# Kernel tuning notes

Measured on AMD Instinct MI355X. Metric: run time of the kernel, lower is better.

The kernel has to match this reference:

```python
import jax, jax.numpy as jnp
import numpy as np

K = 100
TEMPERATURE = 1.0


def setup_inputs() -> dict:
    key = jax.random.key(0)
    k1, k2, k3 = jax.random.split(key, 3)
    student_emb = jax.random.normal(k1, (8, 512, 1500), dtype=jnp.float32)
    teacher_codes = jax.random.randint(k2, (8, 1500), 0, 4096, dtype=jnp.int64)
    codebook = jax.random.normal(k3, (4096, 512), dtype=jnp.float32)
    return {"student_emb": student_emb, "teacher_codes": teacher_codes, "codebook": codebook}


def reference(student_emb, teacher_codes, codebook):
    B, C, T = student_emb.shape
    # flatten tokens: (N, C) with N = B*T
    emb = jnp.transpose(student_emb, (0, 2, 1)).reshape(-1, C)
    codes = teacher_codes.reshape(-1).astype(jnp.int32)

    # Euclidean cdist via the ||a||^2 + ||b||^2 - 2ab expansion (same math as torch.cdist)
    emb_sq = jnp.sum(emb * emb, axis=1, keepdims=True)            # (N,1)
    cb_sq = jnp.sum(codebook * codebook, axis=1)[None, :]         # (1,V)
    d2 = emb_sq + cb_sq - 2.0 * jnp.matmul(emb, codebook.T)       # (N,V)
    distances = jnp.sqrt(jnp.maximum(d2, 0.0))

    # top-k smallest distances
    _, top_k_indices = jax.lax.top_k(-distances, K)               # (N,K)

    # include_correct: replace last candidate with the true code if absent
    correct_in_topk = jnp.any(top_k_indices == codes[:, None], axis=1)
    top_k_indices = top_k_indices.at[:, -1].set(
        jnp.where(correct_in_topk, top_k_indices[:, -1], codes))

    candidate_distances = jnp.take_along_axis(distances, top_k_indices, axis=1)
    logits = -candidate_distances / TEMPERATURE                   # (N,K)

    match = top_k_indices == codes[:, None]
    local_labels = jnp.argmax(match.astype(jnp.int32), axis=1)    # (N,)

    logp = jax.nn.log_softmax(logits, axis=1)
    loss = -jnp.mean(jnp.take_along_axis(logp, local_labels[:, None], axis=1))

    local_predictions = jnp.argmax(logits, axis=-1)
    local_accuracy = jnp.mean((local_predictions == local_labels).astype(jnp.float32))
    global_predictions = jnp.argmin(distances, axis=-1)
    global_accuracy = jnp.mean((global_predictions == codes).astype(jnp.float32))
    correct_in_candidates = jnp.mean(jnp.any(top_k_indices == codes[:, None], axis=1).astype(jnp.float32))

    return loss, local_accuracy, global_accuracy, correct_in_candidates
```

## Files before the change

### kernel.cpp

```cpp
#include <hip/hip_runtime.h>
#include <hip/hip_bf16.h>
#include <cstdint>

#define B_ 8
#define C_ 512
#define T_ 1500
#define N_ (B_*T_)
#define NPAD_ 12032
#define V_ 4096
#define K_ 100
#define BKg 64

typedef unsigned long long u64;
typedef __attribute__((ext_vector_type(8))) short short8;
typedef __attribute__((ext_vector_type(4))) float f32x4;

__device__ __forceinline__ unsigned short f2bf(float x){
    __hip_bfloat16 h = __float2bfloat16(x);
    return __builtin_bit_cast(unsigned short, h);
}
__device__ __forceinline__ unsigned short f2h(float x){
    return __builtin_bit_cast(unsigned short, (_Float16)x);
}
__device__ __forceinline__ float h2fu(unsigned v){
    return (float)__builtin_bit_cast(_Float16, (unsigned short)v);
}

__device__ __forceinline__ void gll16(const unsigned short* g, unsigned short* l){
    __builtin_amdgcn_global_load_lds(
        (const __attribute__((address_space(1))) void*)g,
        (__attribute__((address_space(3))) void*)l, 16, 0, 0);
}

__global__ __launch_bounds__(256) void cbconv_kernel(const float* __restrict__ CB,
                                                     unsigned short* __restrict__ CBh,
                                                     float* __restrict__ csq){
    int wv = threadIdx.x >> 6, lane = threadIdx.x & 63;
    int r = blockIdx.x * 4 + wv;
    const float4* p4 = (const float4*)(CB + (size_t)r * C_);
    ushort4* o4 = (ushort4*)(CBh + (size_t)r * C_);
    float s = 0.f;
    #pragma unroll
    for (int j = 0; j < 2; ++j){
        float4 v = p4[lane + j*64];
        s += v.x*v.x + v.y*v.y + v.z*v.z + v.w*v.w;
        ushort4 h; h.x = f2bf(v.x); h.y = f2bf(v.y); h.z = f2bf(v.z); h.w = f2bf(v.w);
        o4[lane + j*64] = h;
    }
    #pragma unroll
    for (int o = 32; o; o >>= 1) s += __shfl_down(s, o, 64);
    if (lane == 0) csq[r] = s;
}

__global__ __launch_bounds__(256) void transpose_conv_kernel(const float* __restrict__ S,
                                                             unsigned short* __restrict__ embT,
                                                             float* __restrict__ esq){
    __shared__ float tile[32][33];
    __shared__ float psum[8][33];
    int b  = blockIdx.z;
    int c0 = blockIdx.y * 32;
    int t0 = blockIdx.x * 32;
    int tx = threadIdx.x, ty = threadIdx.y;
    #pragma unroll
    for (int r = 0; r < 4; ++r){
        int c = c0 + ty + r*8;
        int t = t0 + tx;
        tile[ty + r*8][tx] = (t < T_) ? S[((size_t)b*C_ + c)*T_ + t] : 0.f;
    }
    __syncthreads();
    float ps = 0.f;
    #pragma unroll
    for (int r = 0; r < 4; ++r){ float v = tile[ty + r*8][tx]; ps += v * v; }
    psum[ty][tx] = ps;
    #pragma unroll
    for (int r = 0; r < 4; ++r){
        int t = t0 + ty + r*8;
        int c = c0 + tx;
        if (t < T_) embT[((size_t)b*T_ + t)*C_ + c] = f2bf(tile[tx][ty + r*8]);
    }
    __syncthreads();
    if (ty == 0){
        int t = t0 + tx;
        if (t < T_){
            float s2 = 0.f;
            #pragma unroll
            for (int w = 0; w < 8; ++w) s2 += psum[w][tx];
            atomicAdd(&esq[b*T_ + t], s2);
        }
    }
}

__global__ __launch_bounds__(256) void gemm_d2h_kernel(
    const unsigned short* __restrict__ A, const unsigned short* __restrict__ Bm,
    const float* __restrict__ esq, const float* __restrict__ csq,
    unsigned short* __restrict__ d2h, int row_lo, int row_hi)
{
    __shared__ unsigned short As[128*BKg];
    __shared__ unsigned short Bs[128*BKg];
    int tid = threadIdx.x, lane = tid & 63, wv = tid >> 6;
    int row0 = row_lo + blockIdx.x * 128;
    int col0 = blockIdx.y * 128;

    int sr = lane >> 3;
    int sk = (lane & 7) * 8;
    int skx = sk ^ (sr * 8);
    const unsigned short* Apg[4]; const unsigned short* Bpg[4];
    unsigned short* Adg[4]; unsigned short* Bdg[4];
    #pragma unroll
    for (int g = 0; g < 4; ++g){
        int r = wv*32 + g*8 + sr;
        int ar = row0 + r; ar = (ar < N_) ? ar : N_-1;
        Apg[g] = A  + (size_t)ar * C_ + skx;
        Bpg[g] = Bm + (size_t)(col0 + r) * C_ + skx;
        Adg[g] = &As[(wv*32 + g*8) * BKg];
        Bdg[g] = &Bs[(wv*32 + g*8) * BKg];
    }

    int wm = (wv >> 1) * 64, wn = (wv & 1) * 64;
    int fr = lane & 15;
    int fk = (lane >> 4) * 8;
    int xo = (fr & 7) * 8;

    f32x4 acc[4][4];
    #pragma unroll
    for (int i = 0; i < 4; ++i)
        #pragma unroll
        for (int j = 0; j < 4; ++j) acc[i][j] = (f32x4){0.f, 0.f, 0.f, 0.f};

    for (int kt = 0; kt < C_/BKg; ++kt){
        int k0 = kt * BKg;
        #pragma unroll
        for (int g = 0; g < 4; ++g) gll16(Apg[g] + k0, Adg[g]);
        #pragma unroll
        for (int g = 0; g < 4; ++g) gll16(Bpg[g] + k0, Bdg[g]);
        __syncthreads();
        #pragma unroll
        for (int kk = 0; kk < 2; ++kk){
            int fo = (fk + kk*32) ^ xo;
            short8 af[4], bf[4];
            #pragma unroll
            for (int i = 0; i < 4; ++i) af[i] = *(const short8*)&As[(wm + i*16 + fr)*BKg + fo];
            #pragma unroll
            for (int j = 0; j < 4; ++j) bf[j] = *(const short8*)&Bs[(wn + j*16 + fr)*BKg + fo];
            #pragma unroll
            for (int i = 0; i < 4; ++i)
                #pragma unroll
                for (int j = 0; j < 4; ++j)
                    acc[i][j] = __builtin_amdgcn_mfma_f32_16x16x32_bf16(af[i], bf[j], acc[i][j], 0, 0, 0);
        }
        __syncthreads();
    }

    int er = (lane >> 4) * 4;
    int ec = lane & 15;
    #pragma unroll
    for (int i = 0; i < 4; ++i){
        #pragma unroll
        for (int r = 0; r < 4; ++r){
            int n = row0 + wm + i*16 + er + r;
            if (n >= row_hi) continue;
            float en = esq[n];
            size_t base = (size_t)(n - row_lo) * V_;
            #pragma unroll
            for (int j = 0; j < 4; ++j){
                int v = col0 + wn + j*16 + ec;
                float d2 = fmaxf(en + csq[v] - 2.f * acc[i][j][r], 0.f);
                d2h[base + v] = f2h(d2);
            }
        }
    }
}

__global__ __launch_bounds__(256, 2) void select_kernel(const unsigned short* __restrict__ d2h,
                                                        const int* __restrict__ codes,
                                                        float2* __restrict__ pairbuf,
                                                        int row_lo, int nrows){
    int tid = threadIdx.x, lane = tid & 63, wv = tid >> 6;
    int lrow = blockIdx.x * 4 + wv;
    if (lrow >= nrows) return;
    int n = row_lo + lrow;
    const uint4* r4 = (const uint4*)(d2h + (size_t)lrow * V_);

    __shared__ unsigned hist[4][256] __attribute__((aligned(16)));
    __shared__ unsigned coll[4][64];
    __shared__ unsigned collcnt[4];

    unsigned p[32];
    #pragma unroll
    for (int j = 0; j < 8; ++j){
        uint4 q = r4[lane + j*64];
        p[4*j] = q.x; p[4*j+1] = q.y; p[4*j+2] = q.z; p[4*j+3] = q.w;
    }
    int code = codes[n];
    unsigned ucode = (unsigned)d2h[(size_t)lrow * V_ + code];

    unsigned cmin = 0xFFFFFFFFu, kmax = 0u;
    #pragma unroll
    for (int m = 0; m < 32; ++m){
        unsigned idx = 8u*(unsigned)lane + 512u*(unsigned)(m>>2) + 2u*(unsigned)(m&3);
        unsigned cl_ = (p[m] << 16) | idx;
        unsigned ch_ = (p[m] & 0xFFFF0000u) | (idx + 1u);
        unsigned cc = (cl_ < ch_) ? cl_ : ch_;
        if (cc < cmin) cmin = cc;
        unsigned lo = p[m] & 0xFFFFu, hi = p[m] >> 16;
        unsigned mm = (lo > hi) ? lo : hi;
        if (mm > kmax) kmax = mm;
    }
    #pragma unroll
    for (int o = 32; o; o >>= 1){
        unsigned a = (unsigned)__shfl_xor((int)cmin, o, 64); if (a < cmin) cmin = a;
        unsigned b = (unsigned)__shfl_xor((int)kmax, o, 64); if (b > kmax) kmax = b;
    }
    unsigned umin = cmin >> 16;
    int idx0 = (int)(cmin & 0xFFFFu);
    float d0 = sqrtf(h2fu(umin));

    unsigned t;
    if (umin == kmax){
        t = umin;
    } else {
        ((uint4*)&hist[wv][0])[lane] = (uint4){0u,0u,0u,0u};
        if (lane == 0) collcnt[wv] = 0u;
        asm volatile("s_waitcnt lgkmcnt(0)" ::: "memory");
        float fmn = h2fu(umin), fmx = h2fu(kmax);
        float invw = 256.0f / (fmx - fmn);
        #pragma unroll
        for (int m = 0; m < 32; ++m){
            int b0 = (int)((h2fu(p[m] & 0xFFFFu) - fmn) * invw); b0 = (b0 > 255) ? 255 : b0;
            int b1 = (int)((h2fu(p[m] >> 16)     - fmn) * invw); b1 = (b1 > 255) ? 255 : b1;
            atomicAdd(&hist[wv][b0], 1u);
            atomicAdd(&hist[wv][b1], 1u);
        }
        asm volatile("s_waitcnt lgkmcnt(0)" ::: "memory");
        uint4 hq = ((uint4*)&hist[wv][0])[lane];
        unsigned lsum = hq.x + hq.y + hq.z + hq.w;
        unsigned inc = lsum;
        #pragma unroll
        for (int o = 1; o < 64; o <<= 1){
            unsigned y = (unsigned)__shfl_up((int)inc, o, 64);
            if (lane >= o) inc += y;
        }
        unsigned e0 = inc - lsum;
        unsigned e1 = e0 + hq.x, e2 = e1 + hq.y, e3 = e2 + hq.z, e4 = e3 + hq.w;
        int sel = -1;
        if      (e0 <= 99u && 99u < e1) sel = 0;
        else if (e1 <= 99u && 99u < e2) sel = 1;
        else if (e2 <= 99u && 99u < e3) sel = 2;
        else if (e3 <= 99u && 99u < e4) sel = 3;
        u64 bal = __ballot(sel >= 0);
        int src = __ffsll(bal) - 1;
        unsigned myBk = (unsigned)(4*lane + (sel < 0 ? 0 : sel));
        unsigned myBase = (sel == 1) ? e1 : (sel == 2) ? e2 : (sel == 3) ? e3 : e0;
        int Bk   = __shfl((int)myBk,   src, 64);
        int base = __shfl((int)myBase, src, 64);
        int rk = 99 - base;
        #pragma unroll
        for (int m = 0; m < 32; ++m){
            unsigned klo = p[m] & 0xFFFFu, khi = p[m] >> 16;
            int b0 = (int)((h2fu(klo) - fmn) * invw); b0 = (b0 > 255) ? 255 : b0;
            int b1 = (int)((h2fu(khi) - fmn) * invw); b1 = (b1 > 255) ? 255 : b1;
            if (b0 == Bk){
                unsigned pos = atomicAdd(&collcnt[wv], 1u);
                if (pos < 64u) coll[wv][pos] = klo;
            }
            if (b1 == Bk){
                unsigned pos = atomicAdd(&collcnt[wv], 1u);
                if (pos < 64u) coll[wv][pos] = khi;
            }
        }
        asm volatile("s_waitcnt lgkmcnt(0)" ::: "memory");
        unsigned bcnt = collcnt[wv];
        if (bcnt <= 64u){
            unsigned w = (lane < (int)bcnt) ? coll[wv][lane] : 0xFFFFFFFFu;
            unsigned wmn = (lane < (int)bcnt) ? w : 0xFFFFFFFFu;
            unsigned wmx = (lane < (int)bcnt) ? w : 0u;
            #pragma unroll
            for (int o = 32; o; o >>= 1){
                unsigned a = (unsigned)__shfl_xor((int)wmn, o, 64); if (a < wmn) wmn = a;
                unsigned b = (unsigned)__shfl_xor((int)wmx, o, 64); if (b > wmx) wmx = b;
            }
            unsigned P;
            if (wmn == wmx) P = wmn;
            else {
                int hb = 31 - __clz((int)(wmn ^ wmx));
                unsigned mask = (1u << (hb+1)) - 1u;
                P = wmn & ~mask;
                for (int b = hb; b >= 0; --b){
                    unsigned cand = P | (1u << b);
                    int c = __popcll(__ballot(w < cand));
                    if (c <= rk) P = cand;
                }
            }
            t = P;
        } else {
            int hb = 31 - __clz((int)(umin ^ kmax));
            unsigned mask = (1u << (hb+1)) - 1u;
            unsigned P = umin & ~mask;
            for (int b = hb; b >= 0; --b){
                unsigned cand = P | (1u << b);
                int c = 0;
                #pragma unroll
                for (int m = 0; m < 32; ++m){
                    c += ((p[m] & 0xFFFFu) < cand) ? 1 : 0;
                    c += ((p[m] >> 16)     < cand) ? 1 : 0;
                }
                #pragma unroll
                for (int o = 32; o; o >>= 1) c += __shfl_xor(c, o, 64);
                if (c <= 99) P = cand;
            }
            t = P;
        }
    }
    float tval = sqrtf(h2fu(t));

    float s = 0.f; int cl = 0;
    #pragma unroll
    for (int m = 0; m < 32; ++m){
        unsigned klo = p[m] & 0xFFFFu, khi = p[m] >> 16;
        if (klo < t){ s += __expf(d0 - sqrtf(h2fu(klo))); cl++; }
        if (khi < t){ s += __expf(d0 - sqrtf(h2fu(khi))); cl++; }
    }
    #pragma unroll
    for (int o = 32; o; o >>= 1){
        s += __shfl_xor(s, o, 64);
        cl += __shfl_xor(cl, o, 64);
    }
    if (lane == 0){
        float S = s + (float)(K_ - cl) * __expf(d0 - tval);
        float dcode = sqrtf(h2fu(ucode));
        if (ucode > t) S += __expf(d0 - dcode) - __expf(d0 - tval);
        float nll = dcode - d0 + __logf(S);
        pairbuf[n] = make_float2(nll, (idx0 == code) ? 1.f : 0.f);
    }
}

__global__ __launch_bounds__(1024) void finalize_kernel(const float2* __restrict__ pair,
                                                        float* __restrict__ out){
    int tid = threadIdx.x;
    float sn = 0.f, sh = 0.f;
    for (int i = tid; i < N_; i += 1024){
        float2 p = pair[i]; sn += p.x; sh += p.y;
    }
    #pragma unroll
    for (int o = 32; o; o >>= 1){ sn += __shfl_down(sn, o, 64); sh += __shfl_down(sh, o, 64); }
    __shared__ float a[16], b[16];
    int wv = tid >> 6, lane = tid & 63;
    if (lane == 0){ a[wv] = sn; b[wv] = sh; }
    __syncthreads();
    if (tid == 0){
        float L = 0.f, H = 0.f;
        #pragma unroll
        for (int i = 0; i < 16; ++i){ L += a[i]; H += b[i]; }
        out[0] = L / (float)N_;
        out[1] = H / (float)N_;
        out[2] = H / (float)N_;
        out[3] = 1.0f;
    }
}

extern "C" void kernel_launch(void* const* d_in, const int* in_sizes, int n_in,
                              void* d_out, int out_size, void* d_ws, size_t ws_size,
                              hipStream_t stream){
    const float* S   = (const float*)d_in[0];
    const int* codes = (const int*)d_in[1];
    const float* CB  = (const float*)d_in[2];
    float* out = (float*)d_out;

    char* w = (char*)d_ws;
    size_t off = 0;
    unsigned short* embT = (unsigned short*)(w + off); off += (size_t)NPAD_ * C_ * 2;
    unsigned short* CBh  = (unsigned short*)(w + off); off += (size_t)V_ * C_ * 2;
    float* csq = (float*)(w + off); off += (size_t)V_ * 4;
    float* esq = (float*)(w + off); off += (size_t)N_ * 4;
    off = (off + 255) & ~(size_t)255;
    float2* pairbuf = (float2*)(w + off); off += (size_t)N_ * 8;
    unsigned short* d2buf = (unsigned short*)(w + off);

    size_t avail = (ws_size > off) ? ws_size - off : 0;
    long maxrows = (long)(avail / ((size_t)V_ * 2));
    int chunk = (maxrows >= N_) ? N_ : (int)maxrows;
    if (chunk < 4) chunk = 4;

    hipMemsetAsync(esq, 0, (size_t)N_ * 4, stream);
    hipLaunchKernelGGL(cbconv_kernel, dim3(V_/4), dim3(256), 0, stream, CB, CBh, csq);
    hipLaunchKernelGGL(transpose_conv_kernel, dim3((T_+31)/32, C_/32, B_), dim3(32, 8), 0, stream,
                       S, embT, esq);

    for (int row_lo = 0; row_lo < N_; row_lo += chunk){
        int row_hi = row_lo + chunk; if (row_hi > N_) row_hi = N_;
        int rows = row_hi - row_lo;
        hipLaunchKernelGGL(gemm_d2h_kernel, dim3((rows + 127)/128, V_/128), dim3(256), 0, stream,
                           embT, CBh, esq, csq, d2buf, row_lo, row_hi);
        hipLaunchKernelGGL(select_kernel, dim3((rows + 3)/4), dim3(256), 0, stream,
                           d2buf, codes, pairbuf, row_lo, rows);
    }
    hipLaunchKernelGGL(finalize_kernel, dim3(1), dim3(1024), 0, stream, pairbuf, out);
}
```

Baseline: 247.5 us.

## Remap GEMM blocks for XCD-aware L2 reuse and shrink K-tile to 32

Replaces the 2D GEMM grid with a 1D grid whose block index is remapped so blocks on the same XCD share row groups of A and half of the codebook columns, aiming to improve L2 hit rates across MI355X's chiplets. It also halves the K-tile from 64 to 32 and adjusts the LDS swizzle accordingly, cutting LDS usage per block, which may raise occupancy. In exchange there are twice as many barrier-separated iterations, and padded blocks must exit early.

```diff
diff --git a/kernel.cpp b/kernel.cpp
--- a/kernel.cpp
+++ b/kernel.cpp
@@ -9,7 +9,6 @@
 #define NPAD_ 12032
 #define V_ 4096
 #define K_ 100
-#define BKg 64
 
 typedef unsigned long long u64;
 typedef __attribute__((ext_vector_type(8))) short short8;
@@ -93,33 +92,38 @@
 __global__ __launch_bounds__(256) void gemm_d2h_kernel(
     const unsigned short* __restrict__ A, const unsigned short* __restrict__ Bm,
     const float* __restrict__ esq, const float* __restrict__ csq,
-    unsigned short* __restrict__ d2h, int row_lo, int row_hi)
+    unsigned short* __restrict__ d2h, int row_lo, int row_hi, int nrb)
 {
-    __shared__ unsigned short As[128*BKg];
-    __shared__ unsigned short Bs[128*BKg];
+    __shared__ unsigned short As[128*32];
+    __shared__ unsigned short Bs[128*32];
     int tid = threadIdx.x, lane = tid & 63, wv = tid >> 6;
-    int row0 = row_lo + blockIdx.x * 128;
-    int col0 = blockIdx.y * 128;
-
-    int sr = lane >> 3;
-    int sk = (lane & 7) * 8;
-    int skx = sk ^ (sr * 8);
-    const unsigned short* Apg[4]; const unsigned short* Bpg[4];
-    unsigned short* Adg[4]; unsigned short* Bdg[4];
-    #pragma unroll
-    for (int g = 0; g < 4; ++g){
-        int r = wv*32 + g*8 + sr;
-        int ar = row0 + r; ar = (ar < N_) ? ar : N_-1;
-        Apg[g] = A  + (size_t)ar * C_ + skx;
-        Bpg[g] = Bm + (size_t)(col0 + r) * C_ + skx;
-        Adg[g] = &As[(wv*32 + g*8) * BKg];
-        Bdg[g] = &Bs[(wv*32 + g*8) * BKg];
-    }
+
+    int b = blockIdx.x;
+    int xcd = b & 7, t = b >> 3;
+    int ul = t >> 4, cb = t & 15;
+    int u = ul * 8 + xcd;
+    int rg = u >> 1, half = u & 1;
+    if (rg >= nrb) return;
+    int row0 = row_lo + rg * 128;
+    int col0 = (half * 16 + cb) * 128;
+
+    int sr = lane >> 2;
+    int skx = ((lane & 3) ^ ((sr >> 1) & 3)) * 8;
+    int ar0 = row0 + wv*32 + sr;       int ar1 = ar0 + 16;
+    int ca0 = (ar0 < N_) ? ar0 : N_-1; int ca1 = (ar1 < N_) ? ar1 : N_-1;
+    const unsigned short* Ap0 = A  + (size_t)ca0 * C_ + skx;
+    const unsigned short* Ap1 = A  + (size_t)ca1 * C_ + skx;
+    const unsigned short* Bp0 = Bm + (size_t)(col0 + wv*32 + sr) * C_ + skx;
+    const unsigned short* Bp1 = Bp0 + (size_t)16 * C_;
+    unsigned short* Ad0 = &As[(wv*32     ) * 32];
+    unsigned short* Ad1 = &As[(wv*32 + 16) * 32];
+    unsigned short* Bd0 = &Bs[(wv*32     ) * 32];
+    unsigned short* Bd1 = &Bs[(wv*32 + 16) * 32];
 
     int wm = (wv >> 1) * 64, wn = (wv & 1) * 64;
     int fr = lane & 15;
     int fk = (lane >> 4) * 8;
-    int xo = (fr & 7) * 8;
+    int fo = fk ^ (((fr >> 1) & 3) * 8);
 
     f32x4 acc[4][4];
     #pragma unroll
@@ -127,27 +131,23 @@
         #pragma unroll
         for (int j = 0; j < 4; ++j) acc[i][j] = (f32x4){0.f, 0.f, 0.f, 0.f};
 
-    for (int kt = 0; kt < C_/BKg; ++kt){
-        int k0 = kt * BKg;
-        #pragma unroll
-        for (int g = 0; g < 4; ++g) gll16(Apg[g] + k0, Adg[g]);
-        #pragma unroll
-        for (int g = 0; g < 4; ++g) gll16(Bpg[g] + k0, Bdg[g]);
+    for (int kt = 0; kt < C_/32; ++kt){
+        int k0 = kt * 32;
+        gll16(Ap0 + k0, Ad0);
+        gll16(Ap1 + k0, Ad1);
+        gll16(Bp0 + k0, Bd0);
+        gll16(Bp1 + k0, Bd1);
         __syncthreads();
-        #pragma unroll
-        for (int kk = 0; kk < 2; ++kk){
-            int fo = (fk + kk*32) ^ xo;
-            short8 af[4], bf[4];
+        short8 af[4], bf[4];
+        #pragma unroll
+        for (int i = 0; i < 4; ++i) af[i] = *(const short8*)&As[(wm + i*16 + fr)*32 + fo];
+        #pragma unroll
+        for (int j = 0; j < 4; ++j) bf[j] = *(const short8*)&Bs[(wn + j*16 + fr)*32 + fo];
+        #pragma unroll
+        for (int i = 0; i < 4; ++i)
             #pragma unroll
-            for (int i = 0; i < 4; ++i) af[i] = *(const short8*)&As[(wm + i*16 + fr)*BKg + fo];
-            #pragma unroll
-            for (int j = 0; j < 4; ++j) bf[j] = *(const short8*)&Bs[(wn + j*16 + fr)*BKg + fo];
-            #pragma unroll
-            for (int i = 0; i < 4; ++i)
-                #pragma unroll
-                for (int j = 0; j < 4; ++j)
-                    acc[i][j] = __builtin_amdgcn_mfma_f32_16x16x32_bf16(af[i], bf[j], acc[i][j], 0, 0, 0);
-        }
+            for (int j = 0; j < 4; ++j)
+                acc[i][j] = __builtin_amdgcn_mfma_f32_16x16x32_bf16(af[i], bf[j], acc[i][j], 0, 0, 0);
         __syncthreads();
     }
 
@@ -389,8 +389,10 @@
     for (int row_lo = 0; row_lo < N_; row_lo += chunk){
         int row_hi = row_lo + chunk; if (row_hi > N_) row_hi = N_;
         int rows = row_hi - row_lo;
-        hipLaunchKernelGGL(gemm_d2h_kernel, dim3((rows + 127)/128, V_/128), dim3(256), 0, stream,
-                           embT, CBh, esq, csq, d2buf, row_lo, row_hi);
+        int nrb = (rows + 127) / 128;
+        int nrbp = (nrb + 7) & ~7;
+        hipLaunchKernelGGL(gemm_d2h_kernel, dim3(nrbp * 32), dim3(256), 0, stream,
+                           embT, CBh, esq, csq, d2buf, row_lo, row_hi, nrb);
         hipLaunchKernelGGL(select_kernel, dim3((rows + 3)/4), dim3(256), 0, stream,
                            d2buf, codes, pairbuf, row_lo, rows);
     }
```

After: 226.2 us. -8.6%, faster.
